# Optimization experiments

Hardware: AMD Instinct MI355X
Metric: run time of the kernel (lower is better)

The kernel has to match this reference:

```python
import jax, jax.numpy as jnp
import numpy as np

B, N, H, FD = 2, 512, 128, 5
NT, SD, L = 3, 4, 3
COPY = 10.0
EPS = 1e-6


def setup_inputs() -> dict:
    key = jax.random.key(0)
    ks = jax.random.split(key, 20)
    node_type = jax.random.randint(ks[0], (B, N, 1), 0, NT).astype(jnp.float32)
    node_state = jax.random.normal(ks[1], (B, N, SD), jnp.float32)
    node_feats = jnp.concatenate([node_type, node_state], axis=-1)  # [B,N,5]
    adj = jax.random.bernoulli(ks[2], 0.05, (B, N, N)).astype(jnp.float32)
    adj = jnp.maximum(adj, adj.transpose(0, 2, 1)) * (1.0 - jnp.eye(N, dtype=jnp.float32))
    scope_node_mask = jax.random.bernoulli(ks[3], 0.5, (B, N)).astype(jnp.float32)
    scope_edge_mask = jax.random.bernoulli(ks[4], 0.5, (B, N, N)).astype(jnp.float32)
    s = 0.02
    p = dict(
        node_feats=node_feats, adj=adj,
        scope_node_mask=scope_node_mask, scope_edge_mask=scope_edge_mask,
        W_in=jax.random.normal(ks[5], (FD, H)) * s, b_in=jnp.zeros((H,)),
        W_mp=jax.random.normal(ks[6], (L, 2 * H, H)) * s, b_mp=jnp.zeros((L, H)),
        Wt1=jax.random.normal(ks[7], (H, H)) * s, bt1=jnp.zeros((H,)),
        Wt2=jax.random.normal(ks[8], (H, NT)) * s, bt2=jnp.zeros((NT,)),
        Ws1=jax.random.normal(ks[9], (H, H)) * s, bs1=jnp.zeros((H,)),
        Ws2=jax.random.normal(ks[10], (H, SD)) * s, bs2=jnp.zeros((SD,)),
        We1=jax.random.normal(ks[11], (4 * H, H)) * s, be1=jnp.zeros((H,)),
        We2=jax.random.normal(ks[12], (H, 3)) * s, be2=jnp.zeros((3,)),
    )
    return p


def _decode_edge_logits(adj, edl, eye):
    probs = jax.nn.softmax(edl, axis=-1)
    p_keep = probs[..., 0]  # EDGE_DELTA_KEEP = 0
    p_add = probs[..., 1]   # EDGE_DELTA_ADD = 1
    cur = (adj > 0.5).astype(edl.dtype)
    p_next = jnp.clip(p_add + p_keep * cur, EPS, 1.0 - EPS)
    el = jnp.log(p_next) - jnp.log1p(-p_next)  # logit
    return jnp.where(eye[None], -1e9, el)


def _forward(node_feats, adj, scope_node_mask, scope_edge_mask,
             W_in, b_in, W_mp, b_mp, Wt1, bt1, Wt2, bt2,
             Ws1, bs1, Ws2, bs2, We1, be1, We2, be2):
    # encoder: input proj + L rounds of [h, adj@h] -> Linear -> ReLU
    h = jax.nn.relu(node_feats @ W_in + b_in)  # [B,N,H]
    for l in range(L):
        msg = jnp.einsum('bij,bjh->bih', adj, h)
        h = jax.nn.relu(jnp.concatenate([h, msg], axis=-1) @ W_mp[l] + b_mp[l])
    # node heads (2-layer MLPs)
    type_local = jax.nn.relu(h @ Wt1 + bt1) @ Wt2 + bt2      # [B,N,NT]
    state_local = jax.nn.relu(h @ Ws1 + bs1) @ Ws2 + bs2     # [B,N,SD]
    # pairwise edge-delta head
    h_i = h[:, :, None, :]
    h_j = h[:, None, :, :]
    pair = jnp.concatenate([
        jnp.broadcast_to(h_i, (B, N, N, H)),
        jnp.broadcast_to(h_j, (B, N, N, H)),
        jnp.abs(h_i - h_j),
        h_i * h_j,
    ], axis=-1)  # [B,N,N,4H]
    edl = jax.nn.relu(pair @ We1 + be1) @ We2 + be2  # [B,N,N,3]
    edl = 0.5 * (edl + edl.transpose(0, 2, 1, 3))
    eye = jnp.eye(N, dtype=bool)
    edl = jnp.where(eye[None, :, :, None], 0.0, edl)
    # merges with copy paths
    cur_type = jnp.clip(node_feats[..., 0].astype(jnp.int32), 0, NT - 1)
    copy_type = jnp.where(jnp.arange(NT) == cur_type[..., None], COPY, -COPY)
    type_full = jnp.where(scope_node_mask[..., None] != 0, type_local, copy_type)
    scope = scope_node_mask[..., None]
    state_full = scope * state_local + (1.0 - scope) * node_feats[..., 1:]
    copy_edl = jnp.broadcast_to(jnp.where(jnp.arange(3) == 0, COPY, -COPY), (B, N, N, 3))
    copy_edl = jnp.where(eye[None, :, :, None], 0.0, copy_edl)
    edl_full = jnp.where(scope_edge_mask[..., None] != 0, edl, copy_edl)
    el_full = _decode_edge_logits(adj, edl_full, eye)
    return type_full, state_full, edl_full, el_full


def reference(node_feats, adj, scope_node_mask, scope_edge_mask,
              W_in, b_in, W_mp, b_mp, Wt1, bt1, Wt2, bt2,
              Ws1, bs1, Ws2, bs2, We1, be1, We2, be2):
    return _forward(node_feats, adj, scope_node_mask, scope_edge_mask,
                    W_in, b_in, W_mp, b_mp, Wt1, bt1, Wt2, bt2,
                    Ws1, bs1, Ws2, bs2, We1, be1, We2, be2)
```

## Files before the change

kernel.cpp:

```cpp
#include <hip/hip_runtime.h>
#include <hip/hip_fp16.h>
#include <math.h>

#define B_ 2
#define N_ 512
#define H_ 128
#define NT_ 3
#define SD_ 4
#define FD_ 5

typedef float f32x4 __attribute__((ext_vector_type(4)));
typedef unsigned int u32x4 __attribute__((ext_vector_type(4)));

#define MFMA4(a0, a1, a2, a3, av, b0, b1, b2, b3) \
    asm("s_nop 1\n\t" \
        "v_mfma_f32_16x16x32_f16 %0, %4, %5, %0\n\t" \
        "v_mfma_f32_16x16x32_f16 %1, %4, %6, %1\n\t" \
        "v_mfma_f32_16x16x32_f16 %2, %4, %7, %2\n\t" \
        "v_mfma_f32_16x16x32_f16 %3, %4, %8, %3" \
        : "+v"(a0), "+v"(a1), "+v"(a2), "+v"(a3) \
        : "v"(av), "v"(b0), "v"(b1), "v"(b2), "v"(b3))

#define MFMA16F(acc, a, b) \
    asm("s_nop 1\n\tv_mfma_f32_16x16x32_f16 %0, %1, %2, %0" \
        : "+v"(acc) : "v"(a), "v"(b))

#define PKMUL(d, a, b) \
    asm("v_pk_mul_f16 %0, %1, %2" : "=v"(d) : "v"(a), "v"(b))
#define PKSUB(d, a, b) \
    asm("v_pk_add_f16 %0, %1, %2 neg_lo:[0,1] neg_hi:[0,1]" \
        : "=v"(d) : "v"(a), "v"(b))
#define CVTPKF16(d, a, b) \
    asm("v_cvt_pkrtz_f16_f32 %0, %1, %2" : "=v"(d) : "v"(a), "v"(b))

static __device__ inline unsigned short f2h(float f) {
    return __half_as_ushort(__float2half(f));
}

__global__ __launch_bounds__(128) void k_input(const float* __restrict__ feats,
                                               const float* __restrict__ W_in,
                                               const float* __restrict__ b_in,
                                               float* __restrict__ hout,
                                               const float* __restrict__ We1,
                                               const float* __restrict__ We2,
                                               unsigned short* __restrict__ wfrag,
                                               unsigned short* __restrict__ wfrag2) {
    int blk = blockIdx.x, tid = threadIdx.x;
    if (blk < B_ * N_) {
        const float* f = feats + (size_t)blk * FD_;
        float acc = b_in[tid];
#pragma unroll
        for (int k = 0; k < FD_; ++k) acc += f[k] * W_in[k * H_ + tid];
        hout[(size_t)blk * H_ + tid] = fmaxf(acc, 0.f);
        return;
    }
    if (blk < B_ * N_ + 32) {
        int t = (blk - B_ * N_) * 128 + tid;
        int lane = t & 63, cg = (t >> 6) & 7, kb = t >> 9;
        int lr = lane & 15, g = lane >> 4;
        int c = cg * 16 + lr;
        unsigned o[4];
#pragma unroll
        for (int p = 0; p < 4; ++p) {
            float a = We1[(size_t)(256 + kb * 32 + 8 * g + 2 * p) * H_ + c];
            float bq = We1[(size_t)(256 + kb * 32 + 8 * g + 2 * p + 1) * H_ + c];
            o[p] = (unsigned)f2h(a) | ((unsigned)f2h(bq) << 16);
        }
        u32x4 v = {o[0], o[1], o[2], o[3]};
        *(u32x4*)(wfrag + (size_t)t * 8) = v;
        return;
    }
    {
        int t = (blk - (B_ * N_ + 32)) * 128 + tid;
        if (t < 256) {
            int kb = t >> 6, lane = t & 63;
            int oc = lane & 15, g = lane >> 4;
            unsigned w[4];
#pragma unroll
            for (int p = 0; p < 4; ++p) {
                int k0 = kb * 32 + g * 8 + 2 * p;
                int k1 = k0 + 1;
                int c0 = ((k0 >> 6) << 6) | ((k0 & 3) << 4) | ((k0 & 63) >> 2);
                int c1 = ((k1 >> 6) << 6) | ((k1 & 3) << 4) | ((k1 & 63) >> 2);
                float v0 = (oc < 3) ? We2[c0 * 3 + oc] : 0.f;
                float v1 = (oc < 3) ? We2[c1 * 3 + oc] : 0.f;
                w[p] = (unsigned)f2h(v0) | ((unsigned)f2h(v1) << 16);
            }
            u32x4 v = {w[0], w[1], w[2], w[3]};
            *(u32x4*)(wfrag2 + (size_t)t * 8) = v;
        }
    }
}

__global__ __launch_bounds__(128) void k_mp(const float* __restrict__ hin,
                                            float* __restrict__ hout,
                                            const float* __restrict__ adj,
                                            const float* __restrict__ Wl,
                                            const float* __restrict__ bl) {
    __shared__ float hi[H_];
    __shared__ float msg[H_];
    __shared__ unsigned short idxs[N_];
    __shared__ float avals[N_];
    __shared__ int cnt2[2];
    int node = blockIdx.x;
    int b = node >> 9;
    int tid = threadIdx.x;
    int w = tid >> 6, lane = tid & 63;
    hi[tid] = hin[(size_t)node * H_ + tid];
    const float* arow = adj + (size_t)node * N_;
    float4 av = ((const float4*)arow)[tid];
    int segbase = w * 256;
    int cum = 0;
#pragma unroll
    for (int q = 0; q < 4; ++q) {
        float a = (&av.x)[q];
        bool pred = (a != 0.f);
        unsigned long long mask = __ballot(pred);
        if (pred) {
            int pos = segbase + cum +
                      (int)__popcll(mask & ((1ull << lane) - 1ull));
            idxs[pos] = (unsigned short)(tid * 4 + q);
            avals[pos] = a;
        }
        cum += (int)__popcll(mask);
    }
    if (lane == 0) cnt2[w] = cum;
    __syncthreads();

    float m = 0.f;
    const float* hb = hin + ((size_t)b * N_) * H_;
    int n0 = cnt2[0], n1 = cnt2[1];
    for (int t = 0; t < n0; ++t)
        m += avals[t] * hb[(size_t)idxs[t] * H_ + tid];
    for (int t = 0; t < n1; ++t)
        m += avals[256 + t] * hb[(size_t)idxs[256 + t] * H_ + tid];
    msg[tid] = m;
    __syncthreads();

    float acc = bl[tid];
#pragma unroll 4
    for (int k = 0; k < H_; ++k) {
        acc += hi[k]  * Wl[(size_t)k * H_ + tid];
        acc += msg[k] * Wl[(size_t)(k + H_) * H_ + tid];
    }
    hout[(size_t)node * H_ + tid] = fmaxf(acc, 0.f);
}

__global__ __launch_bounds__(128) void k_heads(
    const float* __restrict__ h, const float* __restrict__ feats,
    const float* __restrict__ snm,
    const float* __restrict__ Wt1, const float* __restrict__ bt1,
    const float* __restrict__ Wt2, const float* __restrict__ bt2,
    const float* __restrict__ Ws1, const float* __restrict__ bs1,
    const float* __restrict__ Ws2, const float* __restrict__ bs2,
    const float* __restrict__ We1, const float* __restrict__ be1,
    float* __restrict__ Acoef, float* __restrict__ Bcoef,
    unsigned short* __restrict__ hf16,
    float* __restrict__ type_out, float* __restrict__ state_out) {
    __shared__ float hi[H_], hT[H_], hS[H_];
    int node = blockIdx.x, tid = threadIdx.x;
    float hv0 = h[(size_t)node * H_ + tid];
    hi[tid] = hv0;
    hf16[(size_t)node * H_ + tid] = f2h(hv0);
    __syncthreads();
    float at = bt1[tid], as = bs1[tid], aa = be1[tid], ab = 0.f;
#pragma unroll 4
    for (int k = 0; k < H_; ++k) {
        float hv = hi[k];
        at += hv * Wt1[k * H_ + tid];
        as += hv * Ws1[k * H_ + tid];
        aa += hv * We1[k * H_ + tid];
        ab += hv * We1[(k + H_) * H_ + tid];
    }
    hT[tid] = fmaxf(at, 0.f);
    hS[tid] = fmaxf(as, 0.f);
    int c = tid;
    int kp = ((c >> 6) << 6) | ((c & 15) << 2) | ((c >> 4) & 3);
    Acoef[(size_t)node * H_ + kp] = aa;
    Bcoef[(size_t)node * H_ + kp] = ab;
    __syncthreads();
    float sm = snm[node];
    if (tid < NT_) {
        float tl = bt2[tid];
        for (int cc = 0; cc < H_; ++cc) tl += hT[cc] * Wt2[cc * NT_ + tid];
        int ct = (int)feats[(size_t)node * FD_];
        ct = ct < 0 ? 0 : (ct > NT_ - 1 ? NT_ - 1 : ct);
        float cv = (tid == ct) ? 10.f : -10.f;
        type_out[(size_t)node * NT_ + tid] = (sm != 0.f) ? tl : cv;
    }
    if (tid >= 64 && tid < 64 + SD_) {
        int s = tid - 64;
        float sl = bs2[s];
        for (int cc = 0; cc < H_; ++cc) sl += hS[cc] * Ws2[cc * SD_ + s];
        state_out[(size_t)node * SD_ + s] =
            sm * sl + (1.f - sm) * feats[(size_t)node * FD_ + 1 + s];
    }
}

__global__ __launch_bounds__(256, 2) void k_pair2(
    const unsigned short* __restrict__ hf16,
    const float* __restrict__ Acp, const float* __restrict__ Bcp,
    const unsigned short* __restrict__ wfrag,
    const unsigned short* __restrict__ wfrag2,
    const float* __restrict__ be2,
    float* __restrict__ edl_out) {

    __shared__ unsigned short tile[2][128][128];

    int bid = blockIdx.x;
    int b = 0, r = bid;
    if (r >= 1280) { b = 1; r -= 1280; }
    int jtile, i;
    if (r < 128)      { jtile = 0; i = r; }
    else if (r < 384) { jtile = 1; i = r - 128; }
    else if (r < 768) { jtile = 2; i = r - 384; }
    else              { jtile = 3; i = r - 768; }
    int JT0 = jtile << 7;
    int bN = b << 9;

    int tid = threadIdx.x;
    int wave = tid >> 6, lane = tid & 63;
    int jh = wave >> 1, ch = wave & 1;
    int lr = lane & 15, g = lane >> 4;

    u32x4 Bf[4][8];
#pragma unroll
    for (int ct = 0; ct < 4; ++ct)
#pragma unroll
        for (int kb = 0; kb < 8; ++kb)
            Bf[ct][kb] = *(const u32x4*)(wfrag +
                (((size_t)kb * 8 + (ch * 4 + ct)) * 64 + lane) * 8);

    const unsigned short* hirow = hf16 + (size_t)(bN + i) * H_;
    u32x4 him[4];
#pragma unroll
    for (int m = 0; m < 4; ++m)
        him[m] = *(const u32x4*)(hirow + 32 * m + 8 * g);

    f32x4 AcoI = *(const f32x4*)(Acp + (size_t)(bN + i) * H_ + ch * 64 + lr * 4);
    f32x4 BcoI = *(const f32x4*)(Bcp + (size_t)(bN + i) * H_ + ch * 64 + lr * 4);

    char* tb0 = (char*)&tile[0][0][0];
    char* tb1 = (char*)&tile[1][0][0];

#pragma unroll
    for (int jt = 0; jt < 4; ++jt) {
        int jloc0 = jh * 64 + jt * 16;
        const unsigned short* hjp =
            hf16 + (size_t)(bN + JT0 + jloc0 + lr) * H_ + 8 * g;
        u32x4 hjall[4];
#pragma unroll
        for (int m = 0; m < 4; ++m)
            hjall[m] = *(const u32x4*)(hjp + 32 * m);
        f32x4 BcJv[4], AcJv[4];
#pragma unroll
        for (int rr = 0; rr < 4; ++rr) {
            size_t jn = (size_t)(bN + JT0 + jloc0 + 4 * g + rr) * H_ +
                        ch * 64 + lr * 4;
            BcJv[rr] = *(const f32x4*)(Bcp + jn);
            AcJv[rr] = *(const f32x4*)(Acp + jn);
        }

        f32x4 acc0 = {0.f,0.f,0.f,0.f}, acc1 = {0.f,0.f,0.f,0.f};
        f32x4 acc2 = {0.f,0.f,0.f,0.f}, acc3 = {0.f,0.f,0.f,0.f};

#pragma unroll
        for (int m = 0; m < 4; ++m) {
            u32x4 tav, uav;
#pragma unroll
            for (int p = 0; p < 4; ++p) {
                unsigned hip_ = him[m][p], hjp_ = hjall[m][p];
                unsigned u_, d_;
                PKMUL(u_, hip_, hjp_);
                PKSUB(d_, hip_, hjp_);
                uav[p] = u_;
                tav[p] = d_ & 0x7fff7fffu;
            }
            MFMA4(acc0, acc1, acc2, acc3, tav,
                  Bf[0][m], Bf[1][m], Bf[2][m], Bf[3][m]);
            MFMA4(acc0, acc1, acc2, acc3, uav,
                  Bf[0][4 + m], Bf[1][4 + m], Bf[2][4 + m], Bf[3][4 + m]);
        }
        asm("s_nop 7\n\ts_nop 7\n\ts_nop 3"
            : "+v"(acc0), "+v"(acc1), "+v"(acc2), "+v"(acc3));

#pragma unroll
        for (int rr = 0; rr < 4; ++rr) {
            int jloc = jloc0 + 4 * g + rr;
            float h10 = fmaxf(acc0[rr] + AcoI[0] + BcJv[rr][0], 0.f);
            float h11 = fmaxf(acc1[rr] + AcoI[1] + BcJv[rr][1], 0.f);
            float h12 = fmaxf(acc2[rr] + AcoI[2] + BcJv[rr][2], 0.f);
            float h13 = fmaxf(acc3[rr] + AcoI[3] + BcJv[rr][3], 0.f);
            float h20 = fmaxf(acc0[rr] + AcJv[rr][0] + BcoI[0], 0.f);
            float h21 = fmaxf(acc1[rr] + AcJv[rr][1] + BcoI[1], 0.f);
            float h22 = fmaxf(acc2[rr] + AcJv[rr][2] + BcoI[2], 0.f);
            float h23 = fmaxf(acc3[rr] + AcJv[rr][3] + BcoI[3], 0.f);
            unsigned w10, w11, w20, w21;
            CVTPKF16(w10, h10, h11); CVTPKF16(w11, h12, h13);
            CVTPKF16(w20, h20, h21); CVTPKF16(w21, h22, h23);
            int byte = jloc * 256 + ch * 128 + lr * 8;
            byte ^= (jloc & 7) << 4;
            uint2 v1; v1.x = w10; v1.y = w11;
            uint2 v2; v2.x = w20; v2.y = w21;
            *(uint2*)(tb0 + byte) = v1;
            *(uint2*)(tb1 + byte) = v2;
        }
    }

    u32x4 Bf2[4];
#pragma unroll
    for (int kb = 0; kb < 4; ++kb)
        Bf2[kb] = *(const u32x4*)(wfrag2 + ((size_t)kb * 64 + lane) * 8);

    __syncthreads();

    f32x4 pacc0 = {0.f,0.f,0.f,0.f}, pacc1 = {0.f,0.f,0.f,0.f};
    f32x4 pacc2 = {0.f,0.f,0.f,0.f}, pacc3 = {0.f,0.f,0.f,0.f};
#pragma unroll
    for (int p = 0; p < 4; ++p) {
        int f = wave + 4 * p;
        int orient = f >> 3, sub = f & 7;
        char* tb = orient ? tb1 : tb0;
        int jloc = sub * 16 + lr;
#pragma unroll
        for (int kb = 0; kb < 4; ++kb) {
            int byte = jloc * 256 + kb * 64 + g * 16;
            byte ^= (jloc & 7) << 4;
            u32x4 a = *(const u32x4*)(tb + byte);
            if (p == 0)      { MFMA16F(pacc0, a, Bf2[kb]); }
            else if (p == 1) { MFMA16F(pacc1, a, Bf2[kb]); }
            else if (p == 2) { MFMA16F(pacc2, a, Bf2[kb]); }
            else             { MFMA16F(pacc3, a, Bf2[kb]); }
        }
    }
    asm("s_nop 7\n\ts_nop 7\n\ts_nop 3"
        : "+v"(pacc0), "+v"(pacc1), "+v"(pacc2), "+v"(pacc3));
    __syncthreads();

    float* sbuf = (float*)&tile[0][0][0];
    if (lr < 3) {
#pragma unroll
        for (int p = 0; p < 4; ++p) {
            int f = wave + 4 * p;
            int orient = f >> 3, sub = f & 7;
            f32x4 pa = (p == 0) ? pacc0 : (p == 1) ? pacc1
                     : (p == 2) ? pacc2 : pacc3;
#pragma unroll
            for (int rr = 0; rr < 4; ++rr) {
                int jloc = sub * 16 + 4 * g + rr;
                sbuf[((orient << 7) + jloc) * 3 + lr] = pa[rr];
            }
        }
    }
    __syncthreads();

#pragma unroll
    for (int q = 0; q < 2; ++q) {
        int idx = q * 256 + tid;
        if (idx < 384) {
            int jloc = idx / 3, comp = idx - jloc * 3;
            float v = 0.5f * (sbuf[jloc * 3 + comp] +
                              sbuf[(128 + jloc) * 3 + comp]) + be2[comp];
            edl_out[((size_t)(bN + i) * N_ + (JT0 + jloc)) * 3 + comp] = v;
        }
    }
}

__global__ __launch_bounds__(256) void k_tr(float* __restrict__ edl,
                                            float* __restrict__ el,
                                            const float* __restrict__ sem,
                                            const float* __restrict__ adj) {
    __shared__ float ss[3][16][17];
    int tid = threadIdx.x;
    int r = tid >> 4, c = tid & 15;
    int bid = blockIdx.x;
    int b = 0, t = bid;
    if (t >= 528) { b = 1; t -= 528; }
    int J = (int)((sqrtf(8.f * (float)t + 1.f) - 1.f) * 0.5f);
    while ((J + 1) * (J + 2) / 2 <= t) ++J;
    while (J * (J + 1) / 2 > t) --J;
    int I = t - J * (J + 1) / 2;
    int i0 = I * 16, j0 = J * 16;
    int bN = b << 9;

    {
        const float* src = edl + ((size_t)(bN + i0 + r) * N_ + (j0 + c)) * 3;
        ss[0][r][c] = src[0];
        ss[1][r][c] = src[1];
        ss[2][r][c] = src[2];
    }
    __syncthreads();

    for (int pass = 0; pass < 2; ++pass) {
        if (pass == 1 && I == J) break;
        int gi, gj;
        float s0, s1, s2;
        if (I == J) {
            gi = i0 + r; gj = j0 + c;
            int lo = r <= c ? r : c, hi = r <= c ? c : r;
            s0 = ss[0][lo][hi]; s1 = ss[1][lo][hi]; s2 = ss[2][lo][hi];
        } else if (pass == 0) {
            gi = i0 + r; gj = j0 + c;
            s0 = ss[0][r][c]; s1 = ss[1][r][c]; s2 = ss[2][r][c];
        } else {
            gi = j0 + r; gj = i0 + c;
            s0 = ss[0][c][r]; s1 = ss[1][c][r]; s2 = ss[2][c][r];
        }
        size_t p = (size_t)(bN + gi) * N_ + gj;
        if (gi == gj) {
            edl[p * 3 + 0] = 0.f; edl[p * 3 + 1] = 0.f; edl[p * 3 + 2] = 0.f;
            el[p] = -1e9f;
        } else {
            float msk = sem[p];
            float e0 = (msk != 0.f) ? s0 : 10.f;
            float e1 = (msk != 0.f) ? s1 : -10.f;
            float e2 = (msk != 0.f) ? s2 : -10.f;
            edl[p * 3 + 0] = e0; edl[p * 3 + 1] = e1; edl[p * 3 + 2] = e2;
            float a = adj[p];
            float cur = (a > 0.5f) ? 1.f : 0.f;
            float mx = fmaxf(e0, fmaxf(e1, e2));
            float x0 = expf(e0 - mx), x1 = expf(e1 - mx), x2 = expf(e2 - mx);
            float inv = 1.f / (x0 + x1 + x2);
            float pn = x1 * inv + x0 * inv * cur;
            pn = fminf(fmaxf(pn, 1e-6f), 1.f - 1e-6f);
            el[p] = logf(pn) - log1pf(-pn);
        }
    }
}

extern "C" void kernel_launch(void* const* d_in, const int* in_sizes, int n_in,
                              void* d_out, int out_size, void* d_ws,
                              size_t ws_size, hipStream_t stream) {
    const float* feats = (const float*)d_in[0];
    const float* adj   = (const float*)d_in[1];
    const float* snm   = (const float*)d_in[2];
    const float* sem   = (const float*)d_in[3];
    const float* W_in  = (const float*)d_in[4];
    const float* b_in  = (const float*)d_in[5];
    const float* W_mp  = (const float*)d_in[6];
    const float* b_mp  = (const float*)d_in[7];
    const float* Wt1 = (const float*)d_in[8],  *bt1 = (const float*)d_in[9];
    const float* Wt2 = (const float*)d_in[10], *bt2 = (const float*)d_in[11];
    const float* Ws1 = (const float*)d_in[12], *bs1 = (const float*)d_in[13];
    const float* Ws2 = (const float*)d_in[14], *bs2 = (const float*)d_in[15];
    const float* We1 = (const float*)d_in[16], *be1 = (const float*)d_in[17];
    const float* We2 = (const float*)d_in[18], *be2 = (const float*)d_in[19];

    float* out = (float*)d_out;
    float* type_out  = out;
    float* state_out = out + 3072;
    float* edl_out   = out + 7168;
    float* el_out    = out + 7168 + 1572864;

    float* ws = (float*)d_ws;
    float* hA = ws;
    float* hB = ws + 131072;
    float* Bcp = ws + 262144;
    unsigned short* hf16   = (unsigned short*)(ws + 393216);
    unsigned short* wfrag  = (unsigned short*)(ws + 458752);
    unsigned short* wfrag2 = (unsigned short*)(ws + 475136);
    float* Acp = hA;

    k_input<<<B_ * N_ + 34, 128, 0, stream>>>(feats, W_in, b_in, hA,
                                              We1, We2, wfrag, wfrag2);
    k_mp<<<B_ * N_, H_, 0, stream>>>(hA, hB, adj,
                                     W_mp + 0 * 2 * H_ * H_, b_mp + 0 * H_);
    k_mp<<<B_ * N_, H_, 0, stream>>>(hB, hA, adj,
                                     W_mp + 1 * 2 * H_ * H_, b_mp + 1 * H_);
    k_mp<<<B_ * N_, H_, 0, stream>>>(hA, hB, adj,
                                     W_mp + 2 * 2 * H_ * H_, b_mp + 2 * H_);
    k_heads<<<B_ * N_, H_, 0, stream>>>(hB, feats, snm, Wt1, bt1, Wt2, bt2,
                                        Ws1, bs1, Ws2, bs2, We1, be1,
                                        Acp, Bcp, hf16, type_out, state_out);
    k_pair2<<<2560, 256, 0, stream>>>(hf16, Acp, Bcp, wfrag, wfrag2,
                                      be2, edl_out);
    k_tr<<<1056, 256, 0, stream>>>(edl_out, el_out, sem, adj);
}
```

Before: 128.8 us.

## Replace sparse per-node message passing with dense fp16 MFMA tiled kernel

Each message-passing layer now runs as a dense adj@h product plus the concat-linear, both on fp16 MFMA, in 64-node tiles, instead of one block per node doing a sparse gather and a scalar fp32 matvec. Hidden states are kept in fp16 in both row-major and transposed layouts, and the W_mp weights are pre-packed into MFMA fragments in the input kernel. This removes the per-node scalar matvec and its repeated weight reads. In exchange the adjacency is processed densely even though it is about 5% nonzero, only 16 blocks are launched per layer, and the fp16 intermediates lose precision.

Result: slower. 143.1 us (+11.2%).

```diff
diff --git a/kernel.cpp b/kernel.cpp
--- a/kernel.cpp
+++ b/kernel.cpp
@@ -36,26 +36,44 @@
 static __device__ inline unsigned short f2h(float f) {
     return __half_as_ushort(__float2half(f));
 }
+static __device__ inline float h2f(unsigned short u) {
+    return __half2float(__ushort_as_half(u));
+}
 
 __global__ __launch_bounds__(128) void k_input(const float* __restrict__ feats,
                                                const float* __restrict__ W_in,
                                                const float* __restrict__ b_in,
-                                               float* __restrict__ hout,
+                                               unsigned short* __restrict__ h16,
+                                               unsigned short* __restrict__ hT,
                                                const float* __restrict__ We1,
                                                const float* __restrict__ We2,
+                                               const float* __restrict__ W_mp,
                                                unsigned short* __restrict__ wfrag,
-                                               unsigned short* __restrict__ wfrag2) {
+                                               unsigned short* __restrict__ wfrag2,
+                                               unsigned short* __restrict__ wmpf) {
     int blk = blockIdx.x, tid = threadIdx.x;
-    if (blk < B_ * N_) {
-        const float* f = feats + (size_t)blk * FD_;
-        float acc = b_in[tid];
-#pragma unroll
-        for (int k = 0; k < FD_; ++k) acc += f[k] * W_in[k * H_ + tid];
-        hout[(size_t)blk * H_ + tid] = fmaxf(acc, 0.f);
+    if (blk < 128) {
+        int node0 = blk * 8;
+        unsigned short hv[8];
+#pragma unroll
+        for (int n = 0; n < 8; ++n) {
+            const float* f = feats + (size_t)(node0 + n) * FD_;
+            float acc = b_in[tid];
+#pragma unroll
+            for (int k = 0; k < FD_; ++k) acc += f[k] * W_in[k * H_ + tid];
+            acc = fmaxf(acc, 0.f);
+            hv[n] = f2h(acc);
+            h16[(size_t)(node0 + n) * H_ + tid] = hv[n];
+        }
+        u32x4 pk;
+#pragma unroll
+        for (int p = 0; p < 4; ++p)
+            pk[p] = (unsigned)hv[2 * p] | ((unsigned)hv[2 * p + 1] << 16);
+        *(u32x4*)(hT + (size_t)tid * 1024 + node0) = pk;
         return;
     }
-    if (blk < B_ * N_ + 32) {
-        int t = (blk - B_ * N_) * 128 + tid;
+    if (blk < 160) {
+        int t = (blk - 128) * 128 + tid;
         int lane = t & 63, cg = (t >> 6) & 7, kb = t >> 9;
         int lr = lane & 15, g = lane >> 4;
         int c = cg * 16 + lr;
@@ -70,8 +88,8 @@
         *(u32x4*)(wfrag + (size_t)t * 8) = v;
         return;
     }
-    {
-        int t = (blk - (B_ * N_ + 32)) * 128 + tid;
+    if (blk < 162) {
+        int t = (blk - 160) * 128 + tid;
         if (t < 256) {
             int kb = t >> 6, lane = t & 63;
             int oc = lane & 15, g = lane >> 4;
@@ -89,65 +107,166 @@
             u32x4 v = {w[0], w[1], w[2], w[3]};
             *(u32x4*)(wfrag2 + (size_t)t * 8) = v;
         }
-    }
-}
-
-__global__ __launch_bounds__(128) void k_mp(const float* __restrict__ hin,
-                                            float* __restrict__ hout,
-                                            const float* __restrict__ adj,
-                                            const float* __restrict__ Wl,
-                                            const float* __restrict__ bl) {
-    __shared__ float hi[H_];
-    __shared__ float msg[H_];
-    __shared__ unsigned short idxs[N_];
-    __shared__ float avals[N_];
-    __shared__ int cnt2[2];
-    int node = blockIdx.x;
-    int b = node >> 9;
+        return;
+    }
+    {
+        int idx = blk - 162;
+        int l = idx >> 5;
+        int t = (idx & 31) * 128 + tid;
+        int lane = t & 63, cg = (t >> 6) & 7, kb = t >> 9;
+        int lr = lane & 15, g = lane >> 4;
+        int c = cg * 16 + lr;
+        const float* Wl = W_mp + (size_t)l * 256 * H_;
+        unsigned o[4];
+#pragma unroll
+        for (int p = 0; p < 4; ++p) {
+            float a = Wl[(size_t)(kb * 32 + 8 * g + 2 * p) * H_ + c];
+            float bq = Wl[(size_t)(kb * 32 + 8 * g + 2 * p + 1) * H_ + c];
+            o[p] = (unsigned)f2h(a) | ((unsigned)f2h(bq) << 16);
+        }
+        u32x4 v = {o[0], o[1], o[2], o[3]};
+        *(u32x4*)(wmpf + (size_t)l * 32768 + (size_t)t * 8) = v;
+    }
+}
+
+__global__ __launch_bounds__(256) void k_mpm(
+    const unsigned short* __restrict__ h16in,
+    const unsigned short* __restrict__ hTin,
+    unsigned short* __restrict__ h16out,
+    unsigned short* __restrict__ hTout,
+    const float* __restrict__ adj,
+    const unsigned short* __restrict__ wmpf_l,
+    const float* __restrict__ bl,
+    int writeT) {
+    __shared__ unsigned short msgbuf[64][136];
+
+    int blk = blockIdx.x;
+    int b = blk >> 3, mt = blk & 7;
     int tid = threadIdx.x;
-    int w = tid >> 6, lane = tid & 63;
-    hi[tid] = hin[(size_t)node * H_ + tid];
-    const float* arow = adj + (size_t)node * N_;
-    float4 av = ((const float4*)arow)[tid];
-    int segbase = w * 256;
-    int cum = 0;
-#pragma unroll
-    for (int q = 0; q < 4; ++q) {
-        float a = (&av.x)[q];
-        bool pred = (a != 0.f);
-        unsigned long long mask = __ballot(pred);
-        if (pred) {
-            int pos = segbase + cum +
-                      (int)__popcll(mask & ((1ull << lane) - 1ull));
-            idxs[pos] = (unsigned short)(tid * 4 + q);
-            avals[pos] = a;
-        }
-        cum += (int)__popcll(mask);
-    }
-    if (lane == 0) cnt2[w] = cum;
-    __syncthreads();
-
-    float m = 0.f;
-    const float* hb = hin + ((size_t)b * N_) * H_;
-    int n0 = cnt2[0], n1 = cnt2[1];
-    for (int t = 0; t < n0; ++t)
-        m += avals[t] * hb[(size_t)idxs[t] * H_ + tid];
-    for (int t = 0; t < n1; ++t)
-        m += avals[256 + t] * hb[(size_t)idxs[256 + t] * H_ + tid];
-    msg[tid] = m;
-    __syncthreads();
-
-    float acc = bl[tid];
-#pragma unroll 4
-    for (int k = 0; k < H_; ++k) {
-        acc += hi[k]  * Wl[(size_t)k * H_ + tid];
-        acc += msg[k] * Wl[(size_t)(k + H_) * H_ + tid];
-    }
-    hout[(size_t)node * H_ + tid] = fmaxf(acc, 0.f);
+    int wave = tid >> 6, lane = tid & 63;
+    int wm = wave >> 1, wn = wave & 1;
+    int lr = lane & 15, g = lane >> 4;
+    int m_base = mt * 64;
+    int node0 = b * 512 + m_base;
+
+    f32x4 macc[2][4];
+#pragma unroll
+    for (int ms = 0; ms < 2; ++ms)
+#pragma unroll
+        for (int ns = 0; ns < 4; ++ns) macc[ms][ns] = (f32x4){0.f,0.f,0.f,0.f};
+
+#pragma unroll 2
+    for (int ks = 0; ks < 16; ++ks) {
+        u32x4 afr[2];
+#pragma unroll
+        for (int ms = 0; ms < 2; ++ms) {
+            int i_l = m_base + 32 * wm + 16 * ms + lr;
+            const float* ap = adj + ((size_t)(b * 512 + i_l) * 512 + ks * 32 + 8 * g);
+            float4 a0 = *(const float4*)ap;
+            float4 a1 = *(const float4*)(ap + 4);
+            unsigned q0, q1, q2, q3;
+            CVTPKF16(q0, a0.x, a0.y); CVTPKF16(q1, a0.z, a0.w);
+            CVTPKF16(q2, a1.x, a1.y); CVTPKF16(q3, a1.z, a1.w);
+            afr[ms] = (u32x4){q0, q1, q2, q3};
+        }
+        u32x4 bfr[4];
+#pragma unroll
+        for (int ns = 0; ns < 4; ++ns) {
+            int c = 64 * wn + 16 * ns + lr;
+            bfr[ns] = *(const u32x4*)(hTin + (size_t)c * 1024 + b * 512 + ks * 32 + 8 * g);
+        }
+        MFMA4(macc[0][0], macc[0][1], macc[0][2], macc[0][3], afr[0],
+              bfr[0], bfr[1], bfr[2], bfr[3]);
+        MFMA4(macc[1][0], macc[1][1], macc[1][2], macc[1][3], afr[1],
+              bfr[0], bfr[1], bfr[2], bfr[3]);
+    }
+    asm("s_nop 7\n\ts_nop 7\n\ts_nop 3"
+        : "+v"(macc[0][0]), "+v"(macc[0][1]), "+v"(macc[0][2]), "+v"(macc[0][3]),
+          "+v"(macc[1][0]), "+v"(macc[1][1]), "+v"(macc[1][2]), "+v"(macc[1][3]));
+
+#pragma unroll
+    for (int ms = 0; ms < 2; ++ms)
+#pragma unroll
+        for (int ns = 0; ns < 4; ++ns) {
+            int c = 64 * wn + 16 * ns + lr;
+#pragma unroll
+            for (int r = 0; r < 4; ++r) {
+                int m_l = 32 * wm + 16 * ms + 4 * g + r;
+                msgbuf[m_l][c] = f2h(macc[ms][ns][r]);
+            }
+        }
+    __syncthreads();
+
+    f32x4 pacc[2][4];
+#pragma unroll
+    for (int ms = 0; ms < 2; ++ms)
+#pragma unroll
+        for (int ns = 0; ns < 4; ++ns) pacc[ms][ns] = (f32x4){0.f,0.f,0.f,0.f};
+
+#pragma unroll
+    for (int kk = 0; kk < 8; ++kk) {
+        u32x4 afr[2];
+#pragma unroll
+        for (int ms = 0; ms < 2; ++ms) {
+            int m_l = 32 * wm + 16 * ms + lr;
+            if (kk < 4)
+                afr[ms] = *(const u32x4*)(h16in + (size_t)(node0 + m_l) * H_ + kk * 32 + 8 * g);
+            else
+                afr[ms] = *(const u32x4*)&msgbuf[m_l][(kk - 4) * 32 + 8 * g];
+        }
+        u32x4 bfr[4];
+#pragma unroll
+        for (int ns = 0; ns < 4; ++ns)
+            bfr[ns] = *(const u32x4*)(wmpf_l +
+                (((size_t)kk * 8 + (4 * wn + ns)) * 64 + lane) * 8);
+        MFMA4(pacc[0][0], pacc[0][1], pacc[0][2], pacc[0][3], afr[0],
+              bfr[0], bfr[1], bfr[2], bfr[3]);
+        MFMA4(pacc[1][0], pacc[1][1], pacc[1][2], pacc[1][3], afr[1],
+              bfr[0], bfr[1], bfr[2], bfr[3]);
+    }
+    asm("s_nop 7\n\ts_nop 7\n\ts_nop 3"
+        : "+v"(pacc[0][0]), "+v"(pacc[0][1]), "+v"(pacc[0][2]), "+v"(pacc[0][3]),
+          "+v"(pacc[1][0]), "+v"(pacc[1][1]), "+v"(pacc[1][2]), "+v"(pacc[1][3]));
+    __syncthreads();
+
+    float blv[4];
+#pragma unroll
+    for (int ns = 0; ns < 4; ++ns) blv[ns] = bl[64 * wn + 16 * ns + lr];
+
+#pragma unroll
+    for (int ms = 0; ms < 2; ++ms)
+#pragma unroll
+        for (int ns = 0; ns < 4; ++ns) {
+            int c = 64 * wn + 16 * ns + lr;
+            unsigned short hv[4];
+#pragma unroll
+            for (int r = 0; r < 4; ++r) {
+                int m_l = 32 * wm + 16 * ms + 4 * g + r;
+                float v = fmaxf(pacc[ms][ns][r] + blv[ns], 0.f);
+                hv[r] = f2h(v);
+                msgbuf[m_l][c] = hv[r];
+            }
+            if (writeT) {
+                unsigned lo = (unsigned)hv[0] | ((unsigned)hv[1] << 16);
+                unsigned hi = (unsigned)hv[2] | ((unsigned)hv[3] << 16);
+                uint2 pk; pk.x = lo; pk.y = hi;
+                *(uint2*)(hTout + (size_t)c * 1024 + node0 + 32 * wm + 16 * ms + 4 * g) = pk;
+            }
+        }
+    __syncthreads();
+
+    {
+        int row = tid >> 2, cs = (tid & 3) * 32;
+#pragma unroll
+        for (int q = 0; q < 4; ++q) {
+            u32x4 v = *(const u32x4*)&msgbuf[row][cs + q * 8];
+            *(u32x4*)(h16out + (size_t)(node0 + row) * H_ + cs + q * 8) = v;
+        }
+    }
 }
 
 __global__ __launch_bounds__(128) void k_heads(
-    const float* __restrict__ h, const float* __restrict__ feats,
+    const unsigned short* __restrict__ h16, const float* __restrict__ feats,
     const float* __restrict__ snm,
     const float* __restrict__ Wt1, const float* __restrict__ bt1,
     const float* __restrict__ Wt2, const float* __restrict__ bt2,
@@ -155,13 +274,10 @@
     const float* __restrict__ Ws2, const float* __restrict__ bs2,
     const float* __restrict__ We1, const float* __restrict__ be1,
     float* __restrict__ Acoef, float* __restrict__ Bcoef,
-    unsigned short* __restrict__ hf16,
     float* __restrict__ type_out, float* __restrict__ state_out) {
     __shared__ float hi[H_], hT[H_], hS[H_];
     int node = blockIdx.x, tid = threadIdx.x;
-    float hv0 = h[(size_t)node * H_ + tid];
-    hi[tid] = hv0;
-    hf16[(size_t)node * H_ + tid] = f2h(hv0);
+    hi[tid] = h2f(h16[(size_t)node * H_ + tid]);
     __syncthreads();
     float at = bt1[tid], as = bs1[tid], aa = be1[tid], ab = 0.f;
 #pragma unroll 4
@@ -453,26 +569,28 @@
     float* el_out    = out + 7168 + 1572864;
 
     float* ws = (float*)d_ws;
-    float* hA = ws;
-    float* hB = ws + 131072;
-    float* Bcp = ws + 262144;
-    unsigned short* hf16   = (unsigned short*)(ws + 393216);
-    unsigned short* wfrag  = (unsigned short*)(ws + 458752);
-    unsigned short* wfrag2 = (unsigned short*)(ws + 475136);
-    float* Acp = hA;
-
-    k_input<<<B_ * N_ + 34, 128, 0, stream>>>(feats, W_in, b_in, hA,
-                                              We1, We2, wfrag, wfrag2);
-    k_mp<<<B_ * N_, H_, 0, stream>>>(hA, hB, adj,
-                                     W_mp + 0 * 2 * H_ * H_, b_mp + 0 * H_);
-    k_mp<<<B_ * N_, H_, 0, stream>>>(hB, hA, adj,
-                                     W_mp + 1 * 2 * H_ * H_, b_mp + 1 * H_);
-    k_mp<<<B_ * N_, H_, 0, stream>>>(hA, hB, adj,
-                                     W_mp + 2 * 2 * H_ * H_, b_mp + 2 * H_);
-    k_heads<<<B_ * N_, H_, 0, stream>>>(hB, feats, snm, Wt1, bt1, Wt2, bt2,
+    float* Acp = ws;
+    float* Bcp = ws + 131072;
+    unsigned short* h16A = (unsigned short*)(ws + 262144);
+    unsigned short* h16B = (unsigned short*)(ws + 327680);
+    unsigned short* hTA  = (unsigned short*)(ws + 393216);
+    unsigned short* hTB  = (unsigned short*)(ws + 458752);
+    unsigned short* wfrag  = (unsigned short*)(ws + 524288);
+    unsigned short* wfrag2 = (unsigned short*)(ws + 540672);
+    unsigned short* wmpf   = (unsigned short*)(ws + 541696);
+
+    k_input<<<258, 128, 0, stream>>>(feats, W_in, b_in, h16A, hTA,
+                                     We1, We2, W_mp, wfrag, wfrag2, wmpf);
+    k_mpm<<<16, 256, 0, stream>>>(h16A, hTA, h16B, hTB, adj,
+                                  wmpf + 0 * 32768, b_mp + 0 * H_, 1);
+    k_mpm<<<16, 256, 0, stream>>>(h16B, hTB, h16A, hTA, adj,
+                                  wmpf + 1 * 32768, b_mp + 1 * H_, 1);
+    k_mpm<<<16, 256, 0, stream>>>(h16A, hTA, h16B, hTB, adj,
+                                  wmpf + 2 * 32768, b_mp + 2 * H_, 0);
+    k_heads<<<B_ * N_, H_, 0, stream>>>(h16B, feats, snm, Wt1, bt1, Wt2, bt2,
                                         Ws1, bs1, Ws2, bs2, We1, be1,
-                                        Acp, Bcp, hf16, type_out, state_out);
-    k_pair2<<<2560, 256, 0, stream>>>(hf16, Acp, Bcp, wfrag, wfrag2,
+                                        Acp, Bcp, type_out, state_out);
+    k_pair2<<<2560, 256, 0, stream>>>(h16B, Acp, Bcp, wfrag, wfrag2,
                                       be2, edl_out);
     k_tr<<<1056, 256, 0, stream>>>(edl_out, el_out, sem, adj);
 }
```

## Widen message-passing blocks to 256 threads and halve pair-kernel LDS tile

Applied to the files above, without the earlier changes.

The message-passing kernel now uses 256 threads per node. The sparse neighbour gather and the 256-long linear layer are each split across two thread halves and combined through a shared reduction buffer, which adds parallelism per node. The pair kernel processes each 128-column j tile as two 64-column halves, reusing a 32 KB LDS tile instead of 64 KB. The smaller footprint should let more blocks reside per CU, at the cost of extra barriers and a second output-projection pass per block.

Measured after the change: 131.4 us. +2.0%, slower.

```diff
diff --git a/kernel.cpp b/kernel.cpp
--- a/kernel.cpp
+++ b/kernel.cpp
@@ -92,58 +92,63 @@
     }
 }
 
-__global__ __launch_bounds__(128) void k_mp(const float* __restrict__ hin,
+__global__ __launch_bounds__(256) void k_mp(const float* __restrict__ hin,
                                             float* __restrict__ hout,
                                             const float* __restrict__ adj,
                                             const float* __restrict__ Wl,
                                             const float* __restrict__ bl) {
-    __shared__ float hi[H_];
-    __shared__ float msg[H_];
-    __shared__ unsigned short idxs[N_];
-    __shared__ float avals[N_];
-    __shared__ int cnt2[2];
+    __shared__ float xbuf[256];
+    __shared__ unsigned short idxs[512];
+    __shared__ float avals[512];
+    __shared__ float red[256];
+    __shared__ int cnt[4];
     int node = blockIdx.x;
     int b = node >> 9;
     int tid = threadIdx.x;
     int w = tid >> 6, lane = tid & 63;
-    hi[tid] = hin[(size_t)node * H_ + tid];
+    if (tid < 128) xbuf[tid] = hin[(size_t)node * H_ + tid];
     const float* arow = adj + (size_t)node * N_;
-    float4 av = ((const float4*)arow)[tid];
-    int segbase = w * 256;
+    float2 av = ((const float2*)arow)[tid];
     int cum = 0;
 #pragma unroll
-    for (int q = 0; q < 4; ++q) {
-        float a = (&av.x)[q];
+    for (int q2 = 0; q2 < 2; ++q2) {
+        float a = (&av.x)[q2];
         bool pred = (a != 0.f);
         unsigned long long mask = __ballot(pred);
         if (pred) {
-            int pos = segbase + cum +
+            int pos = 128 * w + cum +
                       (int)__popcll(mask & ((1ull << lane) - 1ull));
-            idxs[pos] = (unsigned short)(tid * 4 + q);
+            idxs[pos] = (unsigned short)(2 * tid + q2);
             avals[pos] = a;
         }
         cum += (int)__popcll(mask);
     }
-    if (lane == 0) cnt2[w] = cum;
-    __syncthreads();
-
+    if (lane == 0) cnt[w] = cum;
+    __syncthreads();
+
+    int c = tid & 127, q = tid >> 7;
+    const float* hb = hin + ((size_t)b * N_) * H_;
     float m = 0.f;
-    const float* hb = hin + ((size_t)b * N_) * H_;
-    int n0 = cnt2[0], n1 = cnt2[1];
-    for (int t = 0; t < n0; ++t)
-        m += avals[t] * hb[(size_t)idxs[t] * H_ + tid];
-    for (int t = 0; t < n1; ++t)
-        m += avals[256 + t] * hb[(size_t)idxs[256 + t] * H_ + tid];
-    msg[tid] = m;
-    __syncthreads();
-
-    float acc = bl[tid];
+#pragma unroll
+    for (int s = 0; s < 4; ++s) {
+        int ns = cnt[s];
+        for (int t = q; t < ns; t += 2)
+            m += avals[128 * s + t] * hb[(size_t)idxs[128 * s + t] * H_ + c];
+    }
+    red[q * 128 + c] = m;
+    __syncthreads();
+    if (q == 0) xbuf[128 + c] = red[c] + red[128 + c];
+    __syncthreads();
+
+    float acc = 0.f;
 #pragma unroll 4
-    for (int k = 0; k < H_; ++k) {
-        acc += hi[k]  * Wl[(size_t)k * H_ + tid];
-        acc += msg[k] * Wl[(size_t)(k + H_) * H_ + tid];
-    }
-    hout[(size_t)node * H_ + tid] = fmaxf(acc, 0.f);
+    for (int k = 128 * q; k < 128 * q + 128; ++k)
+        acc += xbuf[k] * Wl[(size_t)k * H_ + c];
+    red[q * 128 + c] = acc;
+    __syncthreads();
+    if (q == 0)
+        hout[(size_t)node * H_ + c] =
+            fmaxf(red[c] + red[128 + c] + bl[c], 0.f);
 }
 
 __global__ __launch_bounds__(128) void k_heads(
@@ -205,7 +210,8 @@
     const float* __restrict__ be2,
     float* __restrict__ edl_out) {
 
-    __shared__ unsigned short tile[2][128][128];
+    __shared__ unsigned short tile[2][64][128];
+    __shared__ float sbuf[2][64][3];
 
     int bid = blockIdx.x;
     int b = 0, r = bid;
@@ -231,6 +237,11 @@
             Bf[ct][kb] = *(const u32x4*)(wfrag +
                 (((size_t)kb * 8 + (ch * 4 + ct)) * 64 + lane) * 8);
 
+    u32x4 Bf2[4];
+#pragma unroll
+    for (int kb = 0; kb < 4; ++kb)
+        Bf2[kb] = *(const u32x4*)(wfrag2 + ((size_t)kb * 64 + lane) * 8);
+
     const unsigned short* hirow = hf16 + (size_t)(bN + i) * H_;
     u32x4 him[4];
 #pragma unroll
@@ -243,125 +254,111 @@
     char* tb0 = (char*)&tile[0][0][0];
     char* tb1 = (char*)&tile[1][0][0];
 
-#pragma unroll
-    for (int jt = 0; jt < 4; ++jt) {
-        int jloc0 = jh * 64 + jt * 16;
-        const unsigned short* hjp =
-            hf16 + (size_t)(bN + JT0 + jloc0 + lr) * H_ + 8 * g;
-        u32x4 hjall[4];
-#pragma unroll
-        for (int m = 0; m < 4; ++m)
-            hjall[m] = *(const u32x4*)(hjp + 32 * m);
-        f32x4 BcJv[4], AcJv[4];
-#pragma unroll
-        for (int rr = 0; rr < 4; ++rr) {
-            size_t jn = (size_t)(bN + JT0 + jloc0 + 4 * g + rr) * H_ +
-                        ch * 64 + lr * 4;
-            BcJv[rr] = *(const f32x4*)(Bcp + jn);
-            AcJv[rr] = *(const f32x4*)(Acp + jn);
-        }
-
-        f32x4 acc0 = {0.f,0.f,0.f,0.f}, acc1 = {0.f,0.f,0.f,0.f};
-        f32x4 acc2 = {0.f,0.f,0.f,0.f}, acc3 = {0.f,0.f,0.f,0.f};
-
-#pragma unroll
-        for (int m = 0; m < 4; ++m) {
-            u32x4 tav, uav;
-#pragma unroll
-            for (int p = 0; p < 4; ++p) {
-                unsigned hip_ = him[m][p], hjp_ = hjall[m][p];
-                unsigned u_, d_;
-                PKMUL(u_, hip_, hjp_);
-                PKSUB(d_, hip_, hjp_);
-                uav[p] = u_;
-                tav[p] = d_ & 0x7fff7fffu;
-            }
-            MFMA4(acc0, acc1, acc2, acc3, tav,
-                  Bf[0][m], Bf[1][m], Bf[2][m], Bf[3][m]);
-            MFMA4(acc0, acc1, acc2, acc3, uav,
-                  Bf[0][4 + m], Bf[1][4 + m], Bf[2][4 + m], Bf[3][4 + m]);
-        }
-        asm("s_nop 7\n\ts_nop 7\n\ts_nop 3"
-            : "+v"(acc0), "+v"(acc1), "+v"(acc2), "+v"(acc3));
-
-#pragma unroll
-        for (int rr = 0; rr < 4; ++rr) {
-            int jloc = jloc0 + 4 * g + rr;
-            float h10 = fmaxf(acc0[rr] + AcoI[0] + BcJv[rr][0], 0.f);
-            float h11 = fmaxf(acc1[rr] + AcoI[1] + BcJv[rr][1], 0.f);
-            float h12 = fmaxf(acc2[rr] + AcoI[2] + BcJv[rr][2], 0.f);
-            float h13 = fmaxf(acc3[rr] + AcoI[3] + BcJv[rr][3], 0.f);
-            float h20 = fmaxf(acc0[rr] + AcJv[rr][0] + BcoI[0], 0.f);
-            float h21 = fmaxf(acc1[rr] + AcJv[rr][1] + BcoI[1], 0.f);
-            float h22 = fmaxf(acc2[rr] + AcJv[rr][2] + BcoI[2], 0.f);
-            float h23 = fmaxf(acc3[rr] + AcJv[rr][3] + BcoI[3], 0.f);
-            unsigned w10, w11, w20, w21;
-            CVTPKF16(w10, h10, h11); CVTPKF16(w11, h12, h13);
-            CVTPKF16(w20, h20, h21); CVTPKF16(w21, h22, h23);
-            int byte = jloc * 256 + ch * 128 + lr * 8;
-            byte ^= (jloc & 7) << 4;
-            uint2 v1; v1.x = w10; v1.y = w11;
-            uint2 v2; v2.x = w20; v2.y = w21;
-            *(uint2*)(tb0 + byte) = v1;
-            *(uint2*)(tb1 + byte) = v2;
-        }
-    }
-
-    u32x4 Bf2[4];
-#pragma unroll
-    for (int kb = 0; kb < 4; ++kb)
-        Bf2[kb] = *(const u32x4*)(wfrag2 + ((size_t)kb * 64 + lane) * 8);
-
-    __syncthreads();
-
-    f32x4 pacc0 = {0.f,0.f,0.f,0.f}, pacc1 = {0.f,0.f,0.f,0.f};
-    f32x4 pacc2 = {0.f,0.f,0.f,0.f}, pacc3 = {0.f,0.f,0.f,0.f};
-#pragma unroll
-    for (int p = 0; p < 4; ++p) {
-        int f = wave + 4 * p;
-        int orient = f >> 3, sub = f & 7;
-        char* tb = orient ? tb1 : tb0;
-        int jloc = sub * 16 + lr;
-#pragma unroll
-        for (int kb = 0; kb < 4; ++kb) {
-            int byte = jloc * 256 + kb * 64 + g * 16;
-            byte ^= (jloc & 7) << 4;
-            u32x4 a = *(const u32x4*)(tb + byte);
-            if (p == 0)      { MFMA16F(pacc0, a, Bf2[kb]); }
-            else if (p == 1) { MFMA16F(pacc1, a, Bf2[kb]); }
-            else if (p == 2) { MFMA16F(pacc2, a, Bf2[kb]); }
-            else             { MFMA16F(pacc3, a, Bf2[kb]); }
-        }
-    }
-    asm("s_nop 7\n\ts_nop 7\n\ts_nop 3"
-        : "+v"(pacc0), "+v"(pacc1), "+v"(pacc2), "+v"(pacc3));
-    __syncthreads();
-
-    float* sbuf = (float*)&tile[0][0][0];
-    if (lr < 3) {
-#pragma unroll
-        for (int p = 0; p < 4; ++p) {
+    for (int jhalf = 0; jhalf < 2; ++jhalf) {
+        int J0 = JT0 + jhalf * 64;
+#pragma unroll
+        for (int jt = 0; jt < 2; ++jt) {
+            int jloc0 = jh * 32 + jt * 16;
+            const unsigned short* hjp =
+                hf16 + (size_t)(bN + J0 + jloc0 + lr) * H_ + 8 * g;
+            u32x4 hjall[4];
+#pragma unroll
+            for (int m = 0; m < 4; ++m)
+                hjall[m] = *(const u32x4*)(hjp + 32 * m);
+            f32x4 BcJv[4], AcJv[4];
+#pragma unroll
+            for (int rr = 0; rr < 4; ++rr) {
+                size_t jn = (size_t)(bN + J0 + jloc0 + 4 * g + rr) * H_ +
+                            ch * 64 + lr * 4;
+                BcJv[rr] = *(const f32x4*)(Bcp + jn);
+                AcJv[rr] = *(const f32x4*)(Acp + jn);
+            }
+
+            f32x4 acc0 = {0.f,0.f,0.f,0.f}, acc1 = {0.f,0.f,0.f,0.f};
+            f32x4 acc2 = {0.f,0.f,0.f,0.f}, acc3 = {0.f,0.f,0.f,0.f};
+
+#pragma unroll
+            for (int m = 0; m < 4; ++m) {
+                u32x4 tav, uav;
+#pragma unroll
+                for (int p = 0; p < 4; ++p) {
+                    unsigned hip_ = him[m][p], hjp_ = hjall[m][p];
+                    unsigned u_, d_;
+                    PKMUL(u_, hip_, hjp_);
+                    PKSUB(d_, hip_, hjp_);
+                    uav[p] = u_;
+                    tav[p] = d_ & 0x7fff7fffu;
+                }
+                MFMA4(acc0, acc1, acc2, acc3, tav,
+                      Bf[0][m], Bf[1][m], Bf[2][m], Bf[3][m]);
+                MFMA4(acc0, acc1, acc2, acc3, uav,
+                      Bf[0][4 + m], Bf[1][4 + m], Bf[2][4 + m], Bf[3][4 + m]);
+            }
+            asm("s_nop 7\n\ts_nop 7\n\ts_nop 3"
+                : "+v"(acc0), "+v"(acc1), "+v"(acc2), "+v"(acc3));
+
+#pragma unroll
+            for (int rr = 0; rr < 4; ++rr) {
+                int jloc = jloc0 + 4 * g + rr;
+                float h10 = fmaxf(acc0[rr] + AcoI[0] + BcJv[rr][0], 0.f);
+                float h11 = fmaxf(acc1[rr] + AcoI[1] + BcJv[rr][1], 0.f);
+                float h12 = fmaxf(acc2[rr] + AcoI[2] + BcJv[rr][2], 0.f);
+                float h13 = fmaxf(acc3[rr] + AcoI[3] + BcJv[rr][3], 0.f);
+                float h20 = fmaxf(acc0[rr] + AcJv[rr][0] + BcoI[0], 0.f);
+                float h21 = fmaxf(acc1[rr] + AcJv[rr][1] + BcoI[1], 0.f);
+                float h22 = fmaxf(acc2[rr] + AcJv[rr][2] + BcoI[2], 0.f);
+                float h23 = fmaxf(acc3[rr] + AcJv[rr][3] + BcoI[3], 0.f);
+                unsigned w10, w11, w20, w21;
+                CVTPKF16(w10, h10, h11); CVTPKF16(w11, h12, h13);
+                CVTPKF16(w20, h20, h21); CVTPKF16(w21, h22, h23);
+                int byte = jloc * 256 + ch * 128 + lr * 8;
+                byte ^= (jloc & 7) << 4;
+                uint2 v1; v1.x = w10; v1.y = w11;
+                uint2 v2; v2.x = w20; v2.y = w21;
+                *(uint2*)(tb0 + byte) = v1;
+                *(uint2*)(tb1 + byte) = v2;
+            }
+        }
+        __syncthreads();
+
+        f32x4 pacc0 = {0.f,0.f,0.f,0.f}, pacc1 = {0.f,0.f,0.f,0.f};
+#pragma unroll
+        for (int p = 0; p < 2; ++p) {
             int f = wave + 4 * p;
-            int orient = f >> 3, sub = f & 7;
-            f32x4 pa = (p == 0) ? pacc0 : (p == 1) ? pacc1
-                     : (p == 2) ? pacc2 : pacc3;
-#pragma unroll
-            for (int rr = 0; rr < 4; ++rr) {
-                int jloc = sub * 16 + 4 * g + rr;
-                sbuf[((orient << 7) + jloc) * 3 + lr] = pa[rr];
-            }
-        }
-    }
-    __syncthreads();
-
-#pragma unroll
-    for (int q = 0; q < 2; ++q) {
-        int idx = q * 256 + tid;
-        if (idx < 384) {
-            int jloc = idx / 3, comp = idx - jloc * 3;
-            float v = 0.5f * (sbuf[jloc * 3 + comp] +
-                              sbuf[(128 + jloc) * 3 + comp]) + be2[comp];
-            edl_out[((size_t)(bN + i) * N_ + (JT0 + jloc)) * 3 + comp] = v;
+            int orient = f >> 2, sub = f & 3;
+            char* tb = orient ? tb1 : tb0;
+            int jloc = sub * 16 + lr;
+#pragma unroll
+            for (int kb = 0; kb < 4; ++kb) {
+                int byte = jloc * 256 + kb * 64 + g * 16;
+                byte ^= (jloc & 7) << 4;
+                u32x4 a = *(const u32x4*)(tb + byte);
+                if (p == 0) { MFMA16F(pacc0, a, Bf2[kb]); }
+                else        { MFMA16F(pacc1, a, Bf2[kb]); }
+            }
+        }
+        asm("s_nop 7\n\ts_nop 7\n\ts_nop 3" : "+v"(pacc0), "+v"(pacc1));
+
+        if (lr < 3) {
+#pragma unroll
+            for (int p = 0; p < 2; ++p) {
+                int f = wave + 4 * p;
+                int orient = f >> 2, sub = f & 3;
+                f32x4 pa = p ? pacc1 : pacc0;
+#pragma unroll
+                for (int rr = 0; rr < 4; ++rr) {
+                    int jloc = sub * 16 + 4 * g + rr;
+                    sbuf[orient][jloc][lr] = pa[rr];
+                }
+            }
+        }
+        __syncthreads();
+
+        if (tid < 192) {
+            int jloc = tid / 3, comp = tid - jloc * 3;
+            float v = 0.5f * (sbuf[0][jloc][comp] + sbuf[1][jloc][comp]) +
+                      be2[comp];
+            edl_out[((size_t)(bN + i) * N_ + (J0 + jloc)) * 3 + comp] = v;
         }
     }
 }
@@ -463,12 +460,12 @@
 
     k_input<<<B_ * N_ + 34, 128, 0, stream>>>(feats, W_in, b_in, hA,
                                               We1, We2, wfrag, wfrag2);
-    k_mp<<<B_ * N_, H_, 0, stream>>>(hA, hB, adj,
-                                     W_mp + 0 * 2 * H_ * H_, b_mp + 0 * H_);
-    k_mp<<<B_ * N_, H_, 0, stream>>>(hB, hA, adj,
-                                     W_mp + 1 * 2 * H_ * H_, b_mp + 1 * H_);
-    k_mp<<<B_ * N_, H_, 0, stream>>>(hA, hB, adj,
-                                     W_mp + 2 * 2 * H_ * H_, b_mp + 2 * H_);
+    k_mp<<<B_ * N_, 256, 0, stream>>>(hA, hB, adj,
+                                      W_mp + 0 * 2 * H_ * H_, b_mp + 0 * H_);
+    k_mp<<<B_ * N_, 256, 0, stream>>>(hB, hA, adj,
+                                      W_mp + 1 * 2 * H_ * H_, b_mp + 1 * H_);
+    k_mp<<<B_ * N_, 256, 0, stream>>>(hA, hB, adj,
+                                      W_mp + 2 * 2 * H_ * H_, b_mp + 2 * H_);
     k_heads<<<B_ * N_, H_, 0, stream>>>(hB, feats, snm, Wt1, bt1, Wt2, bt2,
                                         Ws1, bs1, Ws2, bs2, We1, be1,
                                         Acp, Bcp, hf16, type_out, state_out);
```
